# Optimization experiments

Measured on AMD Instinct MI355X. Metric: run time of the kernel, lower is better.

Reference implementation:

```python
import jax, jax.numpy as jnp
import numpy as np

N_NODES = 100000
N_EDGES = 1600000
IN_DIM = 256
HID = 128
ALPHA = 0.1
K_STEPS = 10


def setup_inputs() -> dict:
    key = jax.random.key(0)
    ks = jax.random.split(key, 10)
    x = jax.random.normal(ks[0], (N_NODES, IN_DIM), dtype=jnp.float32)
    edge_index = jax.random.randint(ks[1], (2, N_EDGES), 0, N_NODES, dtype=jnp.int64)
    s = 0.02
    W1 = jax.random.normal(ks[2], (HID, IN_DIM), dtype=jnp.float32) * s
    b1 = jnp.zeros((HID,), dtype=jnp.float32)
    W2 = jax.random.normal(ks[3], (HID, HID), dtype=jnp.float32) * s
    b2 = jnp.zeros((HID,), dtype=jnp.float32)
    W3 = jax.random.normal(ks[4], (HID, HID), dtype=jnp.float32) * s
    b3 = jnp.zeros((HID,), dtype=jnp.float32)
    Wo = jax.random.normal(ks[5], (1, HID), dtype=jnp.float32) * s
    bo = jnp.zeros((1,), dtype=jnp.float32)
    return {"x": x, "edge_index": edge_index, "W1": W1, "b1": b1,
            "W2": W2, "b2": b2, "W3": W3, "b3": b3, "Wo": Wo, "bo": bo}


def _gcn_norm(edge_index, num_nodes):
    # add self-loops, then symmetric normalization 1/sqrt(deg_i * deg_j)
    loop = jnp.arange(num_nodes, dtype=edge_index.dtype)
    src = jnp.concatenate([edge_index[0], loop])
    dst = jnp.concatenate([edge_index[1], loop])
    ones = jnp.ones(src.shape[0], dtype=jnp.float32)
    deg = jax.ops.segment_sum(ones, dst, num_segments=num_nodes)
    dinv = jnp.where(deg > 0, jax.lax.rsqrt(deg), 0.0)
    norm = dinv[src] * dinv[dst]
    return src, dst, norm


def reference(x, edge_index, W1, b1, W2, b2, W3, b3, Wo, bo):
    # MLP encoder (dropout=0 -> identity in eval)
    h = jax.nn.relu(x @ W1.T + b1)
    h = jax.nn.relu(h @ W2.T + b2)
    h = jax.nn.relu(h @ W3.T + b3)
    # APPNP propagation: h <- (1-alpha) * A_hat h + alpha * h0
    n = x.shape[0]
    src, dst, norm = _gcn_norm(edge_index, n)
    h0 = h
    for _ in range(K_STEPS):
        msg = norm[:, None] * h[src]            # [E+N, HID]
        agg = jax.ops.segment_sum(msg, dst, num_segments=n)
        h = (1.0 - ALPHA) * agg + ALPHA * h0
    out = h @ Wo.T + bo                          # [N, 1]
    return out.squeeze(-1)
```

## Files before the change

kernel.cpp:

```cpp
#include <hip/hip_runtime.h>

#define NN   100000
#define NE   1600000
#define IND  256
#define HIDD 128
#define BCAP 64
#define NPART 196
#define SCAP 10240
#define APITCH 40
#define HPITCH 136

typedef __attribute__((ext_vector_type(8))) short short8v;
typedef __attribute__((ext_vector_type(4))) float f32x4;

__device__ inline float bflo(unsigned w) { return __uint_as_float(w << 16); }
__device__ inline float bfhi(unsigned w) { return __uint_as_float(w & 0xffff0000u); }
__device__ inline unsigned packbf2(float x, float y) {
  unsigned xb = __float_as_uint(x);
  unsigned yb = __float_as_uint(y);
  xb += 0x7fffu + ((xb >> 16) & 1u);
  yb += 0x7fffu + ((yb >> 16) & 1u);
  return (xb >> 16) | (yb & 0xffff0000u);
}
__device__ inline unsigned short bf16r(float x) {
  unsigned b = __float_as_uint(x);
  b += 0x7fffu + ((b >> 16) & 1u);
  return (unsigned short)(b >> 16);
}

__global__ __launch_bounds__(256, 8) void fill_phaseA(
    const int* __restrict__ src, const int* __restrict__ dst,
    int* __restrict__ gcur, unsigned* __restrict__ sbuf)
{
  __shared__ int hist[NPART];
  __shared__ int lofs[NPART];
  const int tid = threadIdx.x;
  const int base = blockIdx.x * 2048;
  for (int i = tid; i < NPART; i += 256) hist[i] = 0;
  __syncthreads();
  int d[8], s[8];
#pragma unroll
  for (int i = 0; i < 8; ++i) {
    int e = base + i * 256 + tid;
    bool v = e < NE;
    d[i] = v ? dst[e] : -1;
    s[i] = v ? src[e] : 0;
    if (v) atomicAdd(&hist[d[i] >> 9], 1);
  }
  __syncthreads();
  for (int i = tid; i < NPART; i += 256)
    lofs[i] = atomicAdd(&gcur[i], hist[i]);
  __syncthreads();
#pragma unroll
  for (int i = 0; i < 8; ++i) {
    if (d[i] >= 0) {
      int p = d[i] >> 9;
      int q = atomicAdd(&lofs[p], 1);
      if (q < SCAP)
        sbuf[(size_t)p * SCAP + q] = ((unsigned)(d[i] & 511) << 17) | (unsigned)s[i];
    }
  }
}

__global__ __launch_bounds__(256, 8) void fill_phaseB(
    const unsigned* __restrict__ sbuf, const int* __restrict__ gcur,
    int* __restrict__ colbuk, int* __restrict__ deg)
{
  __shared__ int lcur[512];
  const int tid = threadIdx.x;
  const int b = blockIdx.x;
  for (int i = tid; i < 512; i += 256) lcur[i] = 0;
  __syncthreads();
  int cnt = min(gcur[b], SCAP);
  const unsigned* sp = sbuf + (size_t)b * SCAP;
  for (int i = tid; i < cnt; i += 256) {
    unsigned u = sp[i];
    int dloc = (int)(u >> 17);
    int s = (int)(u & 0x1FFFFu);
    int pos = atomicAdd(&lcur[dloc], 1);
    if (pos < BCAP) colbuk[(size_t)((b << 9) + dloc) * BCAP + pos] = s;
  }
  __syncthreads();
  for (int i = tid; i < 512; i += 256) {
    int node = (b << 9) + i;
    if (node < NN) deg[node] = lcur[i];
  }
}

__global__ __launch_bounds__(256) void enc_fused(
    const float* __restrict__ x,
    const float* __restrict__ W1, const float* __restrict__ b1,
    const float* __restrict__ W2, const float* __restrict__ b2,
    const float* __restrict__ W3, const float* __restrict__ b3,
    const float* __restrict__ Wo, float* __restrict__ z)
{
  __shared__ unsigned short hbuf[128 * HPITCH];
  __shared__ unsigned short lB[128 * APITCH];
  __shared__ float zsh[2][128];
  unsigned short* lA = hbuf;
  const int tid = threadIdx.x;
  const int lane = tid & 63, wid = tid >> 6;
  const int wr = wid >> 1, wc = wid & 1;
  const int bm = blockIdx.x * 128;
  const int lr = lane & 15, lg = lane >> 4;

  f32x4 acc[4][4];
#pragma unroll
  for (int i = 0; i < 4; ++i)
#pragma unroll
    for (int j = 0; j < 4; ++j) acc[i][j] = (f32x4){0.f, 0.f, 0.f, 0.f};

  for (int k0 = 0; k0 < IND; k0 += 32) {
#pragma unroll
    for (int s0 = 0; s0 < 512; s0 += 256) {
      int s = s0 + tid, rr = s >> 2, g = s & 3;
      int grow = bm + rr;
      float4 v0 = make_float4(0.f, 0.f, 0.f, 0.f), v1 = v0;
      if (grow < NN) {
        const float* ap = x + (size_t)grow * IND + k0 + g * 8;
        v0 = ((const float4*)ap)[0]; v1 = ((const float4*)ap)[1];
      }
      uint4 pk;
      pk.x = packbf2(v0.x, v0.y); pk.y = packbf2(v0.z, v0.w);
      pk.z = packbf2(v1.x, v1.y); pk.w = packbf2(v1.z, v1.w);
      *(uint4*)&lA[rr * APITCH + g * 8] = pk;
      const float* bp = W1 + (size_t)rr * IND + k0 + g * 8;
      float4 w0 = ((const float4*)bp)[0], w1 = ((const float4*)bp)[1];
      uint4 pb;
      pb.x = packbf2(w0.x, w0.y); pb.y = packbf2(w0.z, w0.w);
      pb.z = packbf2(w1.x, w1.y); pb.w = packbf2(w1.z, w1.w);
      *(uint4*)&lB[rr * APITCH + g * 8] = pb;
    }
    __syncthreads();
    {
      short8v a[4], b[4];
#pragma unroll
      for (int i = 0; i < 4; ++i)
        a[i] = *(const short8v*)&lA[(wr * 64 + i * 16 + lr) * APITCH + lg * 8];
#pragma unroll
      for (int j = 0; j < 4; ++j)
        b[j] = *(const short8v*)&lB[(wc * 64 + j * 16 + lr) * APITCH + lg * 8];
#pragma unroll
      for (int i = 0; i < 4; ++i)
#pragma unroll
        for (int j = 0; j < 4; ++j)
          acc[i][j] = __builtin_amdgcn_mfma_f32_16x16x32_bf16(a[i], b[j], acc[i][j], 0, 0, 0);
    }
    __syncthreads();
  }
#pragma unroll
  for (int i = 0; i < 4; ++i)
#pragma unroll
    for (int e = 0; e < 4; ++e) {
      int lrow = wr * 64 + i * 16 + lg * 4 + e;
#pragma unroll
      for (int j = 0; j < 4; ++j) {
        int cc = wc * 64 + j * 16 + lr;
        hbuf[lrow * HPITCH + cc] = bf16r(fmaxf(acc[i][j][e] + b1[cc], 0.f));
      }
    }
  __syncthreads();

#pragma unroll
  for (int i = 0; i < 4; ++i)
#pragma unroll
    for (int j = 0; j < 4; ++j) acc[i][j] = (f32x4){0.f, 0.f, 0.f, 0.f};
  for (int k0 = 0; k0 < HIDD; k0 += 32) {
#pragma unroll
    for (int s0 = 0; s0 < 512; s0 += 256) {
      int s = s0 + tid, rr = s >> 2, g = s & 3;
      const float* bp = W2 + (size_t)rr * HIDD + k0 + g * 8;
      float4 w0 = ((const float4*)bp)[0], w1 = ((const float4*)bp)[1];
      uint4 pb;
      pb.x = packbf2(w0.x, w0.y); pb.y = packbf2(w0.z, w0.w);
      pb.z = packbf2(w1.x, w1.y); pb.w = packbf2(w1.z, w1.w);
      *(uint4*)&lB[rr * APITCH + g * 8] = pb;
    }
    __syncthreads();
    {
      short8v a[4], b[4];
#pragma unroll
      for (int i = 0; i < 4; ++i)
        a[i] = *(const short8v*)&hbuf[(wr * 64 + i * 16 + lr) * HPITCH + k0 + lg * 8];
#pragma unroll
      for (int j = 0; j < 4; ++j)
        b[j] = *(const short8v*)&lB[(wc * 64 + j * 16 + lr) * APITCH + lg * 8];
#pragma unroll
      for (int i = 0; i < 4; ++i)
#pragma unroll
        for (int j = 0; j < 4; ++j)
          acc[i][j] = __builtin_amdgcn_mfma_f32_16x16x32_bf16(a[i], b[j], acc[i][j], 0, 0, 0);
    }
    __syncthreads();
  }
#pragma unroll
  for (int i = 0; i < 4; ++i)
#pragma unroll
    for (int e = 0; e < 4; ++e) {
      int lrow = wr * 64 + i * 16 + lg * 4 + e;
#pragma unroll
      for (int j = 0; j < 4; ++j) {
        int cc = wc * 64 + j * 16 + lr;
        hbuf[lrow * HPITCH + cc] = bf16r(fmaxf(acc[i][j][e] + b2[cc], 0.f));
      }
    }
  __syncthreads();

#pragma unroll
  for (int i = 0; i < 4; ++i)
#pragma unroll
    for (int j = 0; j < 4; ++j) acc[i][j] = (f32x4){0.f, 0.f, 0.f, 0.f};
  for (int k0 = 0; k0 < HIDD; k0 += 32) {
#pragma unroll
    for (int s0 = 0; s0 < 512; s0 += 256) {
      int s = s0 + tid, rr = s >> 2, g = s & 3;
      const float* bp = W3 + (size_t)rr * HIDD + k0 + g * 8;
      float4 w0 = ((const float4*)bp)[0], w1 = ((const float4*)bp)[1];
      uint4 pb;
      pb.x = packbf2(w0.x, w0.y); pb.y = packbf2(w0.z, w0.w);
      pb.z = packbf2(w1.x, w1.y); pb.w = packbf2(w1.z, w1.w);
      *(uint4*)&lB[rr * APITCH + g * 8] = pb;
    }
    __syncthreads();
    {
      short8v a[4], b[4];
#pragma unroll
      for (int i = 0; i < 4; ++i)
        a[i] = *(const short8v*)&hbuf[(wr * 64 + i * 16 + lr) * HPITCH + k0 + lg * 8];
#pragma unroll
      for (int j = 0; j < 4; ++j)
        b[j] = *(const short8v*)&lB[(wc * 64 + j * 16 + lr) * APITCH + lg * 8];
#pragma unroll
      for (int i = 0; i < 4; ++i)
#pragma unroll
        for (int j = 0; j < 4; ++j)
          acc[i][j] = __builtin_amdgcn_mfma_f32_16x16x32_bf16(a[i], b[j], acc[i][j], 0, 0, 0);
    }
    __syncthreads();
  }
  float wv[4];
#pragma unroll
  for (int j = 0; j < 4; ++j) wv[j] = Wo[wc * 64 + j * 16 + lr];
  zsh[tid >> 7][tid & 127] = 0.f;
  __syncthreads();
#pragma unroll
  for (int i = 0; i < 4; ++i)
#pragma unroll
    for (int e = 0; e < 4; ++e) {
      float part = 0.f;
#pragma unroll
      for (int j = 0; j < 4; ++j) {
        int cc = wc * 64 + j * 16 + lr;
        part += fmaxf(acc[i][j][e] + b3[cc], 0.f) * wv[j];
      }
#pragma unroll
      for (int off = 8; off > 0; off >>= 1) part += __shfl_down(part, off, 16);
      if (lr == 0) zsh[wc][wr * 64 + i * 16 + lg * 4 + e] = part;
    }
  __syncthreads();
  if (tid < 128) {
    int row = bm + tid;
    if (row < NN) z[row] = zsh[0][tid] + zsh[1][tid];
  }
}

__global__ void prep_scalar(const int* __restrict__ deg, const float* __restrict__ z,
                            float* __restrict__ dinv, float* __restrict__ va) {
  int i = blockIdx.x * 256 + threadIdx.x;
  if (i < NN) {
    float di = rsqrtf((float)(deg[i] + 1));
    dinv[i] = di;
    va[i] = di * z[i];
  }
}

template<int LAST>
__global__ __launch_bounds__(256, 8) void appnp_sstep(
    const float* __restrict__ vin, const float* __restrict__ z,
    const float* __restrict__ dinv, const int* __restrict__ deg,
    const int* __restrict__ colbuk, float* __restrict__ vout,
    const float* __restrict__ bo, float* __restrict__ out)
{
  int tid = threadIdx.x;
  int sl = tid & 15;
  int node = blockIdx.x * 16 + (tid >> 4);
  if (node >= NN) return;
  int m = min(deg[node], BCAP);
  float val = (sl == 0) ? vin[node] : 0.f;
  for (int j = sl; j < m; j += 16)
    val += vin[colbuk[(size_t)node * BCAP + j]];
#pragma unroll
  for (int off = 8; off > 0; off >>= 1) val += __shfl_down(val, off, 16);
  if (sl == 0) {
    float di = dinv[node];
    float s = 0.9f * di * val + 0.1f * z[node];
    if (LAST) out[node] = s + bo[0];
    else vout[node] = di * s;
  }
}

extern "C" void kernel_launch(void* const* d_in, const int* in_sizes, int n_in,
                              void* d_out, int out_size, void* d_ws, size_t ws_size,
                              hipStream_t stream) {
  const float* x   = (const float*)d_in[0];
  const int*   ei  = (const int*)d_in[1];
  const float* W1  = (const float*)d_in[2];
  const float* b1  = (const float*)d_in[3];
  const float* W2  = (const float*)d_in[4];
  const float* b2  = (const float*)d_in[5];
  const float* W3  = (const float*)d_in[6];
  const float* b3  = (const float*)d_in[7];
  const float* Wo  = (const float*)d_in[8];
  const float* bo  = (const float*)d_in[9];
  float* out = (float*)d_out;

  const int* srcv = ei;
  const int* dstv = ei + NE;

  int*      colbuk = (int*)d_ws;
  unsigned* sbuf   = (unsigned*)(colbuk + (size_t)NN * BCAP);
  int*      gcur   = (int*)(sbuf + (size_t)NPART * SCAP);
  int*      deg    = gcur + NPART;
  float*    dinv   = (float*)(deg + NN);
  float*    zbuf   = dinv + NN;
  float*    va     = zbuf + NN;
  float*    vb     = va + NN;

  hipMemsetAsync(gcur, 0, NPART * 4, stream);

  fill_phaseA<<<(NE + 2047) / 2048, 256, 0, stream>>>(srcv, dstv, gcur, sbuf);
  fill_phaseB<<<NPART, 256, 0, stream>>>(sbuf, gcur, colbuk, deg);

  const int ng = (NN + 127) / 128;
  enc_fused<<<ng, 256, 0, stream>>>(x, W1, b1, W2, b2, W3, b3, Wo, zbuf);

  prep_scalar<<<(NN + 255) / 256, 256, 0, stream>>>(deg, zbuf, dinv, va);

  int ssb = (NN + 15) / 16;
  float* cur = va; float* nxt = vb;
  for (int k = 0; k < 9; ++k) {
    appnp_sstep<0><<<ssb, 256, 0, stream>>>(cur, zbuf, dinv, deg, colbuk,
                                            nxt, nullptr, nullptr);
    float* t = cur; cur = nxt; nxt = t;
  }
  appnp_sstep<1><<<ssb, 256, 0, stream>>>(cur, zbuf, dinv, deg, colbuk,
                                          nullptr, bo, out);
}
```

Measured before the change: 216.3 us.

## Pre-convert MLP weights to bf16 and load MFMA operands directly from global

Adds a small kernel that converts W1, W2 and W3 to bf16 once per call. The encoder then loads MFMA fragments straight from global memory, x converted in registers and weights from the bf16 copies, instead of staging tiles through LDS. This removes the per-k-step LDS stores and barriers and the repeated weight conversion done in every block. In exchange, the x and weight fragment loads are less coalesced and there is no LDS reuse across waves, so the kernel leans on the cache.

```diff
diff --git a/kernel.cpp b/kernel.cpp
--- a/kernel.cpp
+++ b/kernel.cpp
@@ -7,14 +7,11 @@
 #define BCAP 64
 #define NPART 196
 #define SCAP 10240
-#define APITCH 40
 #define HPITCH 136
 
 typedef __attribute__((ext_vector_type(8))) short short8v;
 typedef __attribute__((ext_vector_type(4))) float f32x4;
 
-__device__ inline float bflo(unsigned w) { return __uint_as_float(w << 16); }
-__device__ inline float bfhi(unsigned w) { return __uint_as_float(w & 0xffff0000u); }
 __device__ inline unsigned packbf2(float x, float y) {
   unsigned xb = __float_as_uint(x);
   unsigned yb = __float_as_uint(y);
@@ -26,6 +23,18 @@
   unsigned b = __float_as_uint(x);
   b += 0x7fffu + ((b >> 16) & 1u);
   return (unsigned short)(b >> 16);
+}
+
+__global__ void wcvt_all(const float* __restrict__ W1, const float* __restrict__ W2,
+                         const float* __restrict__ W3, unsigned* __restrict__ W1b,
+                         unsigned* __restrict__ W2b, unsigned* __restrict__ W3b) {
+  int i = blockIdx.x * 256 + threadIdx.x;
+  const float* src; unsigned* dst; int off;
+  if (i < 16384)      { src = W1; dst = W1b; off = i; }
+  else if (i < 24576) { src = W2; dst = W2b; off = i - 16384; }
+  else                { src = W3; dst = W3b; off = i - 24576; }
+  float2 v = ((const float2*)src)[off];
+  dst[off] = packbf2(v.x, v.y);
 }
 
 __global__ __launch_bounds__(256, 8) void fill_phaseA(
@@ -89,15 +98,13 @@
 
 __global__ __launch_bounds__(256) void enc_fused(
     const float* __restrict__ x,
-    const float* __restrict__ W1, const float* __restrict__ b1,
-    const float* __restrict__ W2, const float* __restrict__ b2,
-    const float* __restrict__ W3, const float* __restrict__ b3,
+    const unsigned short* __restrict__ W1b, const float* __restrict__ b1,
+    const unsigned short* __restrict__ W2b, const float* __restrict__ b2,
+    const unsigned short* __restrict__ W3b, const float* __restrict__ b3,
     const float* __restrict__ Wo, float* __restrict__ z)
 {
   __shared__ unsigned short hbuf[128 * HPITCH];
-  __shared__ unsigned short lB[128 * APITCH];
   __shared__ float zsh[2][128];
-  unsigned short* lA = hbuf;
   const int tid = threadIdx.x;
   const int lane = tid & 63, wid = tid >> 6;
   const int wr = wid >> 1, wc = wid & 1;
@@ -111,42 +118,28 @@
     for (int j = 0; j < 4; ++j) acc[i][j] = (f32x4){0.f, 0.f, 0.f, 0.f};
 
   for (int k0 = 0; k0 < IND; k0 += 32) {
-#pragma unroll
-    for (int s0 = 0; s0 < 512; s0 += 256) {
-      int s = s0 + tid, rr = s >> 2, g = s & 3;
-      int grow = bm + rr;
-      float4 v0 = make_float4(0.f, 0.f, 0.f, 0.f), v1 = v0;
+    short8v a[4], b[4];
+#pragma unroll
+    for (int i = 0; i < 4; ++i) {
+      int grow = bm + wr * 64 + i * 16 + lr;
+      uint4 pk = make_uint4(0u, 0u, 0u, 0u);
       if (grow < NN) {
-        const float* ap = x + (size_t)grow * IND + k0 + g * 8;
-        v0 = ((const float4*)ap)[0]; v1 = ((const float4*)ap)[1];
+        const float* ap = x + (size_t)grow * IND + k0 + lg * 8;
+        float4 v0 = ((const float4*)ap)[0];
+        float4 v1 = ((const float4*)ap)[1];
+        pk.x = packbf2(v0.x, v0.y); pk.y = packbf2(v0.z, v0.w);
+        pk.z = packbf2(v1.x, v1.y); pk.w = packbf2(v1.z, v1.w);
       }
-      uint4 pk;
-      pk.x = packbf2(v0.x, v0.y); pk.y = packbf2(v0.z, v0.w);
-      pk.z = packbf2(v1.x, v1.y); pk.w = packbf2(v1.z, v1.w);
-      *(uint4*)&lA[rr * APITCH + g * 8] = pk;
-      const float* bp = W1 + (size_t)rr * IND + k0 + g * 8;
-      float4 w0 = ((const float4*)bp)[0], w1 = ((const float4*)bp)[1];
-      uint4 pb;
-      pb.x = packbf2(w0.x, w0.y); pb.y = packbf2(w0.z, w0.w);
-      pb.z = packbf2(w1.x, w1.y); pb.w = packbf2(w1.z, w1.w);
-      *(uint4*)&lB[rr * APITCH + g * 8] = pb;
-    }
-    __syncthreads();
-    {
-      short8v a[4], b[4];
-#pragma unroll
-      for (int i = 0; i < 4; ++i)
-        a[i] = *(const short8v*)&lA[(wr * 64 + i * 16 + lr) * APITCH + lg * 8];
+      a[i] = *(short8v*)&pk;
+    }
+#pragma unroll
+    for (int j = 0; j < 4; ++j)
+      b[j] = *(const short8v*)&W1b[(size_t)(wc * 64 + j * 16 + lr) * IND + k0 + lg * 8];
+#pragma unroll
+    for (int i = 0; i < 4; ++i)
 #pragma unroll
       for (int j = 0; j < 4; ++j)
-        b[j] = *(const short8v*)&lB[(wc * 64 + j * 16 + lr) * APITCH + lg * 8];
-#pragma unroll
-      for (int i = 0; i < 4; ++i)
-#pragma unroll
-        for (int j = 0; j < 4; ++j)
-          acc[i][j] = __builtin_amdgcn_mfma_f32_16x16x32_bf16(a[i], b[j], acc[i][j], 0, 0, 0);
-    }
-    __syncthreads();
+        acc[i][j] = __builtin_amdgcn_mfma_f32_16x16x32_bf16(a[i], b[j], acc[i][j], 0, 0, 0);
   }
 #pragma unroll
   for (int i = 0; i < 4; ++i)
@@ -166,33 +159,20 @@
 #pragma unroll
     for (int j = 0; j < 4; ++j) acc[i][j] = (f32x4){0.f, 0.f, 0.f, 0.f};
   for (int k0 = 0; k0 < HIDD; k0 += 32) {
-#pragma unroll
-    for (int s0 = 0; s0 < 512; s0 += 256) {
-      int s = s0 + tid, rr = s >> 2, g = s & 3;
-      const float* bp = W2 + (size_t)rr * HIDD + k0 + g * 8;
-      float4 w0 = ((const float4*)bp)[0], w1 = ((const float4*)bp)[1];
-      uint4 pb;
-      pb.x = packbf2(w0.x, w0.y); pb.y = packbf2(w0.z, w0.w);
-      pb.z = packbf2(w1.x, w1.y); pb.w = packbf2(w1.z, w1.w);
-      *(uint4*)&lB[rr * APITCH + g * 8] = pb;
-    }
-    __syncthreads();
-    {
-      short8v a[4], b[4];
-#pragma unroll
-      for (int i = 0; i < 4; ++i)
-        a[i] = *(const short8v*)&hbuf[(wr * 64 + i * 16 + lr) * HPITCH + k0 + lg * 8];
+    short8v a[4], b[4];
+#pragma unroll
+    for (int i = 0; i < 4; ++i)
+      a[i] = *(const short8v*)&hbuf[(wr * 64 + i * 16 + lr) * HPITCH + k0 + lg * 8];
+#pragma unroll
+    for (int j = 0; j < 4; ++j)
+      b[j] = *(const short8v*)&W2b[(size_t)(wc * 64 + j * 16 + lr) * HIDD + k0 + lg * 8];
+#pragma unroll
+    for (int i = 0; i < 4; ++i)
 #pragma unroll
       for (int j = 0; j < 4; ++j)
-        b[j] = *(const short8v*)&lB[(wc * 64 + j * 16 + lr) * APITCH + lg * 8];
-#pragma unroll
-      for (int i = 0; i < 4; ++i)
-#pragma unroll
-        for (int j = 0; j < 4; ++j)
-          acc[i][j] = __builtin_amdgcn_mfma_f32_16x16x32_bf16(a[i], b[j], acc[i][j], 0, 0, 0);
-    }
-    __syncthreads();
-  }
+        acc[i][j] = __builtin_amdgcn_mfma_f32_16x16x32_bf16(a[i], b[j], acc[i][j], 0, 0, 0);
+  }
+  __syncthreads();
 #pragma unroll
   for (int i = 0; i < 4; ++i)
 #pragma unroll
@@ -211,32 +191,18 @@
 #pragma unroll
     for (int j = 0; j < 4; ++j) acc[i][j] = (f32x4){0.f, 0.f, 0.f, 0.f};
   for (int k0 = 0; k0 < HIDD; k0 += 32) {
-#pragma unroll
-    for (int s0 = 0; s0 < 512; s0 += 256) {
-      int s = s0 + tid, rr = s >> 2, g = s & 3;
-      const float* bp = W3 + (size_t)rr * HIDD + k0 + g * 8;
-      float4 w0 = ((const float4*)bp)[0], w1 = ((const float4*)bp)[1];
-      uint4 pb;
-      pb.x = packbf2(w0.x, w0.y); pb.y = packbf2(w0.z, w0.w);
-      pb.z = packbf2(w1.x, w1.y); pb.w = packbf2(w1.z, w1.w);
-      *(uint4*)&lB[rr * APITCH + g * 8] = pb;
-    }
-    __syncthreads();
-    {
-      short8v a[4], b[4];
-#pragma unroll
-      for (int i = 0; i < 4; ++i)
-        a[i] = *(const short8v*)&hbuf[(wr * 64 + i * 16 + lr) * HPITCH + k0 + lg * 8];
+    short8v a[4], b[4];
+#pragma unroll
+    for (int i = 0; i < 4; ++i)
+      a[i] = *(const short8v*)&hbuf[(wr * 64 + i * 16 + lr) * HPITCH + k0 + lg * 8];
+#pragma unroll
+    for (int j = 0; j < 4; ++j)
+      b[j] = *(const short8v*)&W3b[(size_t)(wc * 64 + j * 16 + lr) * HIDD + k0 + lg * 8];
+#pragma unroll
+    for (int i = 0; i < 4; ++i)
 #pragma unroll
       for (int j = 0; j < 4; ++j)
-        b[j] = *(const short8v*)&lB[(wc * 64 + j * 16 + lr) * APITCH + lg * 8];
-#pragma unroll
-      for (int i = 0; i < 4; ++i)
-#pragma unroll
-        for (int j = 0; j < 4; ++j)
-          acc[i][j] = __builtin_amdgcn_mfma_f32_16x16x32_bf16(a[i], b[j], acc[i][j], 0, 0, 0);
-    }
-    __syncthreads();
+        acc[i][j] = __builtin_amdgcn_mfma_f32_16x16x32_bf16(a[i], b[j], acc[i][j], 0, 0, 0);
   }
   float wv[4];
 #pragma unroll
@@ -325,14 +291,21 @@
   float*    zbuf   = dinv + NN;
   float*    va     = zbuf + NN;
   float*    vb     = va + NN;
+  unsigned* W1b    = (unsigned*)(vb + NN);
+  unsigned* W2b    = W1b + 16384;
+  unsigned* W3b    = W2b + 8192;
 
   hipMemsetAsync(gcur, 0, NPART * 4, stream);
+
+  wcvt_all<<<128, 256, 0, stream>>>(W1, W2, W3, W1b, W2b, W3b);
 
   fill_phaseA<<<(NE + 2047) / 2048, 256, 0, stream>>>(srcv, dstv, gcur, sbuf);
   fill_phaseB<<<NPART, 256, 0, stream>>>(sbuf, gcur, colbuk, deg);
 
   const int ng = (NN + 127) / 128;
-  enc_fused<<<ng, 256, 0, stream>>>(x, W1, b1, W2, b2, W3, b3, Wo, zbuf);
+  enc_fused<<<ng, 256, 0, stream>>>(x, (unsigned short*)W1b, b1,
+                                    (unsigned short*)W2b, b2,
+                                    (unsigned short*)W3b, b3, Wo, zbuf);
 
   prep_scalar<<<(NN + 255) / 256, 256, 0, stream>>>(deg, zbuf, dinv, va);
 
```

New measurement: 235.9 us. +9.0%, slower.
